# Performance work log

Hardware: AMD Instinct MI355X
Metric: run time of the kernel (lower is better)

## Reference

```python
import jax, jax.numpy as jnp
import numpy as np

N, E, F, H, G, C = 50000, 800000, 768, 256, 512, 2  # H = nhid*2 (nhid=128), G graphs, C classes
NHID = 128


def setup_inputs() -> dict:
    key = jax.random.key(0)
    ks = jax.random.split(key, 18)
    s = 0.05
    x = jax.random.normal(ks[0], (N, F), jnp.float32)
    edge_index = jax.random.randint(ks[1], (2, E), 0, N, dtype=jnp.int32)
    # sorted batch vector; every graph non-empty so the 'first node per graph' gather is valid
    batch = ((jnp.arange(N) * G) // N).astype(jnp.int32)
    return {
        "x": x,
        "edge_index": edge_index,
        "batch": batch,
        # GATConv 1 (in=F, out=H, heads=1)
        "W1": jax.random.normal(ks[2], (F, H), jnp.float32) * s,
        "as1": jax.random.normal(ks[3], (H,), jnp.float32) * s,
        "ad1": jax.random.normal(ks[4], (H,), jnp.float32) * s,
        "b1": jnp.zeros((H,), jnp.float32),
        # GATConv 2 (in=H, out=H)
        "W2": jax.random.normal(ks[5], (H, H), jnp.float32) * s,
        "as2": jax.random.normal(ks[6], (H,), jnp.float32) * s,
        "ad2": jax.random.normal(ks[7], (H,), jnp.float32) * s,
        "b2": jnp.zeros((H,), jnp.float32),
        # fc0: num_features -> nhid (news branch)
        "W0": jax.random.normal(ks[8], (F, NHID), jnp.float32) * s,
        "b0": jnp.zeros((NHID,), jnp.float32),
        # fc1: 2*nhid -> nhid (used twice, as in the source)
        "Wf1": jax.random.normal(ks[9], (H, NHID), jnp.float32) * s,
        "bf1": jnp.zeros((NHID,), jnp.float32),
        # fc2: nhid -> num_classes
        "Wf2": jax.random.normal(ks[10], (NHID, C), jnp.float32) * s,
        "bf2": jnp.zeros((C,), jnp.float32),
    }


def _gat(x, src, dst, W, a_s, a_d, b):
    # PyG GATConv, heads=1, concat=True, negative_slope=0.2, self-loops pre-appended to src/dst.
    h = x @ W                                   # [N, H]
    e = jax.nn.leaky_relu((h @ a_s)[src] + (h @ a_d)[dst], 0.2)  # [E+N]
    m = jax.ops.segment_max(e, dst, num_segments=N)
    ex = jnp.exp(e - m[dst])                    # stable segment softmax numerator
    denom = jax.ops.segment_sum(ex, dst, num_segments=N)
    agg = jax.ops.segment_sum(ex[:, None] * h[src], dst, num_segments=N)  # [N, H]
    return agg / denom[:, None] + b


def reference(x, edge_index, batch, W1, as1, ad1, b1, W2, as2, ad2, b2, W0, b0, Wf1, bf1, Wf2, bf2):
    loop = jnp.arange(N, dtype=edge_index.dtype)
    src = jnp.concatenate([edge_index[0], loop])  # add self-loops (PyG default)
    dst = jnp.concatenate([edge_index[1], loop])
    h = jax.nn.selu(_gat(x, src, dst, W1, as1, ad1, b1))
    h = jax.nn.selu(_gat(h, src, dst, W2, as2, ad2, b2))
    # global mean pool over graphs
    cnt = jax.ops.segment_sum(jnp.ones((N,), h.dtype), batch, num_segments=G)
    pooled = jax.nn.selu(jax.ops.segment_sum(h, batch, num_segments=G) / cnt[:, None])
    z = jax.nn.selu(pooled @ Wf1 + bf1)
    # dropout(p=0.5) in eval mode -> identity
    # concat branch: first node of each graph (news root)
    first_idx = jax.ops.segment_min(jnp.arange(N), batch, num_segments=G)
    news = jax.nn.relu(x[first_idx] @ W0 + b0)
    z = jnp.concatenate([z, news], axis=1)       # [G, 2*nhid]
    z = jax.nn.relu(z @ Wf1 + bf1)
    return jax.nn.log_softmax(z @ Wf2 + bf2, axis=-1)
```

## Files before the change

### kernel.cpp

```cpp
#include <hip/hip_runtime.h>
#include <hip/hip_bf16.h>
#include <cstdint>
#include <cstddef>

#define NN 50000
#define EE 800000
#define FF 768
#define HH 256
#define GG 512
#define CC 2
#define NHIDD 128
#define ETOT (EE + NN)
#define NCHUNK 49

typedef __attribute__((ext_vector_type(8))) short bf16x8;
typedef __attribute__((ext_vector_type(4))) float f32x4;
typedef __attribute__((ext_vector_type(8))) unsigned short us8;

__device__ __forceinline__ float b2f(unsigned short u){
  union { float f; uint32_t i; } v; v.i = ((uint32_t)u) << 16; return v.f;
}
__device__ __forceinline__ unsigned short f2b(float f){
  uint32_t u = __float_as_uint(f);
  uint32_t r = (u + 0x7fffu + ((u >> 16) & 1u)) >> 16;
  return (unsigned short)r;
}
__device__ __forceinline__ float selu_f(float x){
  const float lam = 1.0507009873554805f, alp = 1.6732632423543772f;
  return x > 0.f ? lam * x : lam * alp * (__expf(x) - 1.f);
}

__global__ __launch_bounds__(256) void swizzleW(const float* __restrict__ W,
                                                unsigned short* __restrict__ Wsw, int K){
  int i = blockIdx.x * 256 + threadIdx.x;
  if (i < K * HH){
    int k = i / HH, n = i % HH;
    Wsw[(size_t)(k >> 5) * 8192 + n * 32 + (k & 31)] = f2b(W[i]);
  }
}

__global__ __launch_bounds__(256) void zero_deg(int* deg){
  int i = blockIdx.x * 256 + threadIdx.x;
  if (i < NN) deg[i] = 0;
}

__global__ __launch_bounds__(256) void deg_kernel(const int* __restrict__ dstA, int* __restrict__ deg){
  int i = blockIdx.x * 256 + threadIdx.x;
  if (i < ETOT){
    int d = (i < EE) ? dstA[i] : (i - EE);
    atomicAdd(&deg[d], 1);
  }
}

__global__ __launch_bounds__(256) void scanA(const int* __restrict__ deg, int* __restrict__ bsum){
  __shared__ int red[256];
  int c = blockIdx.x, tid = threadIdx.x;
  int base = c * 1024 + tid * 4;
  int s = 0;
#pragma unroll
  for (int j = 0; j < 4; j++){ int idx = base + j; if (idx < NN) s += deg[idx]; }
  red[tid] = s; __syncthreads();
  for (int off = 128; off > 0; off >>= 1){
    if (tid < off) red[tid] += red[tid + off];
    __syncthreads();
  }
  if (tid == 0) bsum[c] = red[0];
}

__global__ void scanB(int* bsum){
  if (threadIdx.x == 0){
    int run = 0;
    for (int i = 0; i < NCHUNK; i++){ int v = bsum[i]; bsum[i] = run; run += v; }
  }
}

__global__ __launch_bounds__(256) void scanC(const int* __restrict__ deg, const int* __restrict__ bsum,
                                             int* __restrict__ row_ptr, int* __restrict__ fill_ptr){
  __shared__ int ts[256];
  int c = blockIdx.x, tid = threadIdx.x;
  int base = c * 1024 + tid * 4;
  int v[4]; int s = 0;
#pragma unroll
  for (int j = 0; j < 4; j++){ int idx = base + j; v[j] = (idx < NN) ? deg[idx] : 0; s += v[j]; }
  ts[tid] = s; __syncthreads();
  for (int off = 1; off < 256; off <<= 1){
    int add = (tid >= off) ? ts[tid - off] : 0;
    __syncthreads();
    ts[tid] += add;
    __syncthreads();
  }
  int run = ts[tid] - s + bsum[c];
#pragma unroll
  for (int j = 0; j < 4; j++){
    int idx = base + j;
    if (idx < NN){ row_ptr[idx] = run; fill_ptr[idx] = run; }
    run += v[j];
  }
  if (c == 0 && tid == 0) row_ptr[NN] = ETOT;
}

__global__ __launch_bounds__(256) void fill_kernel(const int* __restrict__ srcA, const int* __restrict__ dstA,
                                                   int* __restrict__ fill_ptr, int* __restrict__ csr_src){
  int i = blockIdx.x * 256 + threadIdx.x;
  if (i < ETOT){
    int s = (i < EE) ? srcA[i] : (i - EE);
    int d = (i < EE) ? dstA[i] : (i - EE);
    int pos = atomicAdd(&fill_ptr[d], 1);
    csr_src[pos] = s;
  }
}

template<int K, bool AF32, int MINW>
__global__ __launch_bounds__(256, MINW) void gemm_mfma(const void* __restrict__ Ap,
                                                 const unsigned short* __restrict__ Wsw,
                                                 unsigned short* __restrict__ out, int M){
  constexpr int KP = K + 8;
  __shared__ unsigned short Al[32][KP];
  const int tid = threadIdx.x;
  const int m0 = blockIdx.x * 32;
  const int lane = tid & 63, w = tid >> 6;
  const int koff = (lane >> 4) * 8;
  const int arow = lane & 15;
  const int nrow = w * 64 + (lane & 15);

  f32x4 acc[2][4];
#pragma unroll
  for (int rt = 0; rt < 2; rt++)
#pragma unroll
    for (int ct = 0; ct < 4; ct++) acc[rt][ct] = (f32x4){0.f, 0.f, 0.f, 0.f};

  constexpr int C8 = K / 8;
  constexpr int ROUNDS = (32 * C8) / 256;
#pragma unroll
  for (int j = 0; j < ROUNDS; j++){
    int q = j * 256 + tid;
    int row = q / C8, c8 = q - row * C8;
    int gm = m0 + row;
    us8 v;
    if (gm < M){
      if (AF32){
        const float* Af = (const float*)Ap;
        const float4* p = (const float4*)&Af[(size_t)gm * K + c8 * 8];
        float4 f0 = p[0], f1 = p[1];
        v[0] = f2b(f0.x); v[1] = f2b(f0.y); v[2] = f2b(f0.z); v[3] = f2b(f0.w);
        v[4] = f2b(f1.x); v[5] = f2b(f1.y); v[6] = f2b(f1.z); v[7] = f2b(f1.w);
      } else {
        v = *(const us8*)&((const unsigned short*)Ap)[(size_t)gm * K + c8 * 8];
      }
    } else {
      v = (us8){0,0,0,0,0,0,0,0};
    }
    *(us8*)&Al[row][c8 * 8] = v;
  }

  const unsigned short* bbase = Wsw + ((size_t)nrow * 32 + koff);
  bf16x8 bcur[2][4];
#pragma unroll
  for (int k2 = 0; k2 < 2; k2++)
#pragma unroll
    for (int ct = 0; ct < 4; ct++)
      bcur[k2][ct] = *(const bf16x8*)(bbase + (size_t)k2 * 8192 + ct * 512);

  __syncthreads();

  constexpr int NIT = K / 64;
  for (int ks = 0; ks < NIT; ks++){
    bf16x8 bnext[2][4];
    if (ks + 1 < NIT){
#pragma unroll
      for (int k2 = 0; k2 < 2; k2++)
#pragma unroll
        for (int ct = 0; ct < 4; ct++)
          bnext[k2][ct] = *(const bf16x8*)(bbase + (size_t)((ks + 1) * 2 + k2) * 8192 + ct * 512);
    }
    bf16x8 af[2][2];
#pragma unroll
    for (int k2 = 0; k2 < 2; k2++)
#pragma unroll
      for (int rt = 0; rt < 2; rt++)
        af[k2][rt] = *(const bf16x8*)&Al[rt * 16 + arow][ks * 64 + k2 * 32 + koff];
#pragma unroll
    for (int k2 = 0; k2 < 2; k2++)
#pragma unroll
      for (int rt = 0; rt < 2; rt++)
#pragma unroll
        for (int ct = 0; ct < 4; ct++)
          acc[rt][ct] = __builtin_amdgcn_mfma_f32_16x16x32_bf16(af[k2][rt], bcur[k2][ct], acc[rt][ct], 0, 0, 0);
    if (ks + 1 < NIT){
#pragma unroll
      for (int k2 = 0; k2 < 2; k2++)
#pragma unroll
        for (int ct = 0; ct < 4; ct++) bcur[k2][ct] = bnext[k2][ct];
    }
  }

#pragma unroll
  for (int rt = 0; rt < 2; rt++){
    int mbase = m0 + rt * 16 + (lane >> 4) * 4;
#pragma unroll
    for (int r = 0; r < 4; r++){
      int m = mbase + r;
      if (m < M){
        size_t ro = (size_t)m * HH + w * 64 + (lane & 15);
        out[ro + 0]  = f2b(acc[rt][0][r]);
        out[ro + 16] = f2b(acc[rt][1][r]);
        out[ro + 32] = f2b(acc[rt][2][r]);
        out[ro + 48] = f2b(acc[rt][3][r]);
      }
    }
  }
}

__global__ __launch_bounds__(256) void alsald_kernel(const unsigned short* __restrict__ h,
    const float* __restrict__ a_s, const float* __restrict__ a_d,
    float* __restrict__ als, float* __restrict__ ald){
  int node = blockIdx.x * 4 + (threadIdx.x >> 6);
  int lane = threadIdx.x & 63;
  if (node >= NN) return;
  ushort4 hv = *(const ushort4*)&h[(size_t)node * HH + lane * 4];
  float4 as4 = *(const float4*)&a_s[lane * 4];
  float4 ad4 = *(const float4*)&a_d[lane * 4];
  float h0 = b2f(hv.x), h1 = b2f(hv.y), h2 = b2f(hv.z), h3 = b2f(hv.w);
  float s = h0 * as4.x + h1 * as4.y + h2 * as4.z + h3 * as4.w;
  float d = h0 * ad4.x + h1 * ad4.y + h2 * ad4.z + h3 * ad4.w;
  for (int off = 32; off > 0; off >>= 1){ s += __shfl_xor(s, off); d += __shfl_xor(d, off); }
  if (lane == 0){ als[node] = s; ald[node] = d; }
}

__global__ __launch_bounds__(256) void agg_wave(const unsigned short* __restrict__ h,
    const float* __restrict__ als, const float* __restrict__ ald,
    const int* __restrict__ row_ptr, const int* __restrict__ csr_src,
    const float* __restrict__ bias, unsigned short* __restrict__ outp){
  int node = blockIdx.x * 4 + (threadIdx.x >> 6);
  int lane = threadIdx.x & 63;
  if (node >= NN) return;
  int base = row_ptr[node];
  int deg  = row_ptr[node + 1] - base;
  float aldd = ald[node];
  float den = 0.f;
  float a0 = 0.f, a1 = 0.f, a2 = 0.f, a3 = 0.f;
  const size_t fo = (size_t)lane * 4;
  for (int p0 = 0; p0 < deg; p0 += 64){
    int cnt = min(64, deg - p0);
    float ev = 0.f; int s = 0;
    if (lane < cnt){
      s = csr_src[base + p0 + lane];
      float v = als[s] + aldd;
      v = v > 0.f ? v : 0.2f * v;
      ev = __expf(v);
    }
    den += ev;
    int j = 0;
    for (; j + 2 <= cnt; j += 2){
      float e0 = __shfl(ev, j), e1 = __shfl(ev, j + 1);
      int s0 = __shfl(s, j), s1 = __shfl(s, j + 1);
      ushort4 g0 = *(const ushort4*)&h[(size_t)s0 * HH + fo];
      ushort4 g1 = *(const ushort4*)&h[(size_t)s1 * HH + fo];
      a0 += e0 * b2f(g0.x) + e1 * b2f(g1.x);
      a1 += e0 * b2f(g0.y) + e1 * b2f(g1.y);
      a2 += e0 * b2f(g0.z) + e1 * b2f(g1.z);
      a3 += e0 * b2f(g0.w) + e1 * b2f(g1.w);
    }
    for (; j < cnt; j++){
      float e0 = __shfl(ev, j); int s0 = __shfl(s, j);
      ushort4 g0 = *(const ushort4*)&h[(size_t)s0 * HH + fo];
      a0 += e0 * b2f(g0.x); a1 += e0 * b2f(g0.y); a2 += e0 * b2f(g0.z); a3 += e0 * b2f(g0.w);
    }
  }
  for (int off = 32; off > 0; off >>= 1) den += __shfl_xor(den, off);
  float inv = 1.f / den;
  float4 b4 = *(const float4*)&bias[fo];
  ushort4 o;
  o.x = f2b(selu_f(a0 * inv + b4.x));
  o.y = f2b(selu_f(a1 * inv + b4.y));
  o.z = f2b(selu_f(a2 * inv + b4.z));
  o.w = f2b(selu_f(a3 * inv + b4.w));
  *(ushort4*)&outp[(size_t)node * HH + fo] = o;
}

__global__ __launch_bounds__(256) void first_kernel(const int* __restrict__ batch, int* __restrict__ first_idx){
  int n = blockIdx.x * 256 + threadIdx.x;
  if (n < NN){
    int b = batch[n];
    if (n == 0 || batch[n - 1] != b) first_idx[b] = n;
  }
  if (blockIdx.x == 0 && threadIdx.x == 0) first_idx[GG] = NN;
}

__global__ __launch_bounds__(256) void pool_kernel(const unsigned short* __restrict__ x3,
    const int* __restrict__ first_idx, float* __restrict__ pooled){
  int g = blockIdx.x, f = threadIdx.x;
  int s = first_idx[g], e = first_idx[g + 1];
  float acc = 0.f;
  for (int n = s; n < e; n++) acc += b2f(x3[(size_t)n * HH + f]);
  pooled[g * HH + f] = selu_f(acc / (float)(e - s));
}

__global__ __launch_bounds__(128) void z1_kernel(const float* __restrict__ pooled,
    const float* __restrict__ Wf1, const float* __restrict__ bf1,
    float* __restrict__ z1){
  __shared__ float pr[HH];
  int g = blockIdx.x, t = threadIdx.x;
  pr[t] = pooled[g * HH + t];
  pr[t + 128] = pooled[g * HH + t + 128];
  __syncthreads();
  float acc = 0.f;
  for (int k = 0; k < HH; k++) acc += pr[k] * Wf1[k * NHIDD + t];
  z1[g * NHIDD + t] = selu_f(acc + bf1[t]);
}

__global__ __launch_bounds__(128) void news_kernel(const float* __restrict__ x,
    const int* __restrict__ first_idx, const float* __restrict__ W0,
    const float* __restrict__ b0, float* __restrict__ znews){
  __shared__ float xr[FF];
  int g = blockIdx.x, t = threadIdx.x;
  int root = first_idx[g];
  for (int k = t; k < FF; k += 128) xr[k] = x[(size_t)root * FF + k];
  __syncthreads();
  float acc = 0.f;
  for (int k = 0; k < FF; k++) acc += xr[k] * W0[k * NHIDD + t];
  acc += b0[t];
  znews[g * NHIDD + t] = acc > 0.f ? acc : 0.f;
}

__global__ __launch_bounds__(128) void final_kernel(const float* __restrict__ z1,
    const float* __restrict__ znews, const float* __restrict__ Wf1,
    const float* __restrict__ bf1, const float* __restrict__ Wf2,
    const float* __restrict__ bf2, float* __restrict__ out){
  __shared__ float zc[HH];
  __shared__ float l0s[2], l1s[2];
  int g = blockIdx.x, t = threadIdx.x;
  zc[t] = z1[g * NHIDD + t];
  zc[NHIDD + t] = znews[g * NHIDD + t];
  __syncthreads();
  float acc = 0.f;
  for (int k = 0; k < HH; k++) acc += zc[k] * Wf1[k * NHIDD + t];
  float z2 = acc + bf1[t]; z2 = z2 > 0.f ? z2 : 0.f;
  float p0 = z2 * Wf2[t * CC + 0];
  float p1 = z2 * Wf2[t * CC + 1];
  for (int off = 32; off > 0; off >>= 1){ p0 += __shfl_xor(p0, off); p1 += __shfl_xor(p1, off); }
  int lane = t & 63, wid = t >> 6;
  if (lane == 0){ l0s[wid] = p0; l1s[wid] = p1; }
  __syncthreads();
  if (t == 0){
    float l0 = l0s[0] + l0s[1] + bf2[0];
    float l1 = l1s[0] + l1s[1] + bf2[1];
    float mx = fmaxf(l0, l1);
    float lse = mx + logf(__expf(l0 - mx) + __expf(l1 - mx));
    out[g * CC + 0] = l0 - lse;
    out[g * CC + 1] = l1 - lse;
  }
}

extern "C" void kernel_launch(void* const* d_in, const int* in_sizes, int n_in,
                              void* d_out, int out_size, void* d_ws, size_t ws_size,
                              hipStream_t stream){
  const float* x          = (const float*)d_in[0];
  const int* edge_index   = (const int*)d_in[1];
  const int* batch        = (const int*)d_in[2];
  const float* W1  = (const float*)d_in[3];
  const float* as1 = (const float*)d_in[4];
  const float* ad1 = (const float*)d_in[5];
  const float* b1  = (const float*)d_in[6];
  const float* W2  = (const float*)d_in[7];
  const float* as2 = (const float*)d_in[8];
  const float* ad2 = (const float*)d_in[9];
  const float* b2  = (const float*)d_in[10];
  const float* W0  = (const float*)d_in[11];
  const float* b0  = (const float*)d_in[12];
  const float* Wf1 = (const float*)d_in[13];
  const float* bf1 = (const float*)d_in[14];
  const float* Wf2 = (const float*)d_in[15];
  const float* bf2 = (const float*)d_in[16];
  float* out = (float*)d_out;

  char* w = (char*)d_ws;
  size_t off = 0;
  auto alloc = [&](size_t bytes){ size_t o = off; off += (bytes + 255) & ~(size_t)255; return o; };
  unsigned short* h    = (unsigned short*)(w + alloc((size_t)NN * HH * 2));
  unsigned short* x2   = (unsigned short*)(w + alloc((size_t)NN * HH * 2));
  unsigned short* Wsw1 = (unsigned short*)(w + alloc((size_t)FF * HH * 2));
  unsigned short* Wsw2 = (unsigned short*)(w + alloc((size_t)HH * HH * 2));
  float* als     = (float*)(w + alloc((size_t)NN * 4));
  float* ald     = (float*)(w + alloc((size_t)NN * 4));
  int*   deg     = (int*)(w + alloc((size_t)NN * 4));
  int*   row_ptr = (int*)(w + alloc((size_t)(NN + 1) * 4));
  int*   fillp   = (int*)(w + alloc((size_t)NN * 4));
  int*   csr_src = (int*)(w + alloc((size_t)ETOT * 4));
  int*   bsum    = (int*)(w + alloc(64 * 4));
  int*   firsti  = (int*)(w + alloc((size_t)(GG + 1) * 4));
  float* pooled  = (float*)(w + alloc((size_t)GG * HH * 4));
  float* z1      = (float*)(w + alloc((size_t)GG * NHIDD * 4));
  float* znews   = (float*)(w + alloc((size_t)GG * NHIDD * 4));

  const int* srcA = edge_index;
  const int* dstA = edge_index + EE;

  swizzleW<<<(FF * HH + 255) / 256, 256, 0, stream>>>(W1, Wsw1, FF);
  swizzleW<<<(HH * HH + 255) / 256, 256, 0, stream>>>(W2, Wsw2, HH);

  zero_deg<<<(NN + 255) / 256, 256, 0, stream>>>(deg);
  deg_kernel<<<(ETOT + 255) / 256, 256, 0, stream>>>(dstA, deg);
  scanA<<<NCHUNK, 256, 0, stream>>>(deg, bsum);
  scanB<<<1, 64, 0, stream>>>(bsum);
  scanC<<<NCHUNK, 256, 0, stream>>>(deg, bsum, row_ptr, fillp);
  fill_kernel<<<(ETOT + 255) / 256, 256, 0, stream>>>(srcA, dstA, fillp, csr_src);

  const int gemm_grid = (NN + 31) / 32;
  gemm_mfma<FF, true, 3><<<gemm_grid, 256, 0, stream>>>((const void*)x, Wsw1, h, NN);
  alsald_kernel<<<(NN + 3) / 4, 256, 0, stream>>>(h, as1, ad1, als, ald);
  agg_wave<<<(NN + 3) / 4, 256, 0, stream>>>(h, als, ald, row_ptr, csr_src, b1, x2);
  gemm_mfma<HH, false, 4><<<gemm_grid, 256, 0, stream>>>((const void*)x2, Wsw2, h, NN);
  alsald_kernel<<<(NN + 3) / 4, 256, 0, stream>>>(h, as2, ad2, als, ald);
  agg_wave<<<(NN + 3) / 4, 256, 0, stream>>>(h, als, ald, row_ptr, csr_src, b2, x2);
  first_kernel<<<(NN + 255) / 256, 256, 0, stream>>>(batch, firsti);
  pool_kernel<<<GG, 256, 0, stream>>>(x2, firsti, pooled);
  z1_kernel<<<GG, 128, 0, stream>>>(pooled, Wf1, bf1, z1);
  news_kernel<<<GG, 128, 0, stream>>>(x, firsti, W0, b0, znews);
  final_kernel<<<GG, 128, 0, stream>>>(z1, znews, Wf1, bf1, Wf2, bf2, out);
}
```

Baseline: 627.0 us.

## Fuse attention-logit dot products into GEMM epilogue and use direct-to-LDS loads

Folds the per-node a_s/a_d dot products into the MFMA GEMM epilogue through shuffle and LDS reductions, which removes the separate alsald kernel and its re-read of h. The A-tile load now goes straight from global memory to LDS via global_load_lds with an XOR swizzle in place of padding. To allow this, x is converted to bf16 in a separate pre-pass kernel. That pass writes and re-reads a 77MB bf16 copy in exchange for the fp32 reads that used to happen inside the GEMM, and the second GEMM's occupancy hint drops from 4 to 3.

```diff
diff --git a/kernel.cpp b/kernel.cpp
--- a/kernel.cpp
+++ b/kernel.cpp
@@ -30,6 +30,21 @@
   return x > 0.f ? lam * x : lam * alp * (__expf(x) - 1.f);
 }
 
+__device__ __forceinline__ void gload_lds16(const unsigned short* g, unsigned short* l){
+  __builtin_amdgcn_global_load_lds((const __attribute__((address_space(1))) void*)g,
+                                   (__attribute__((address_space(3))) void*)l, 16, 0, 0);
+}
+
+__global__ __launch_bounds__(256) void xbf_kernel(const float* __restrict__ x, unsigned short* __restrict__ xb){
+  size_t i = ((size_t)blockIdx.x * 256 + threadIdx.x) * 8;
+  float4 f0 = *(const float4*)&x[i];
+  float4 f1 = *(const float4*)&x[i + 4];
+  us8 v;
+  v[0] = f2b(f0.x); v[1] = f2b(f0.y); v[2] = f2b(f0.z); v[3] = f2b(f0.w);
+  v[4] = f2b(f1.x); v[5] = f2b(f1.y); v[6] = f2b(f1.z); v[7] = f2b(f1.w);
+  *(us8*)&xb[i] = v;
+}
+
 __global__ __launch_bounds__(256) void swizzleW(const float* __restrict__ W,
                                                 unsigned short* __restrict__ Wsw, int K){
   int i = blockIdx.x * 256 + threadIdx.x;
@@ -110,12 +125,14 @@
   }
 }
 
-template<int K, bool AF32, int MINW>
-__global__ __launch_bounds__(256, MINW) void gemm_mfma(const void* __restrict__ Ap,
+template<int K, int MINW>
+__global__ __launch_bounds__(256, MINW) void gemm_mfma(const unsigned short* __restrict__ A,
                                                  const unsigned short* __restrict__ Wsw,
-                                                 unsigned short* __restrict__ out, int M){
-  constexpr int KP = K + 8;
-  __shared__ unsigned short Al[32][KP];
+                                                 const float* __restrict__ a_s, const float* __restrict__ a_d,
+                                                 unsigned short* __restrict__ out,
+                                                 float* __restrict__ als, float* __restrict__ ald, int M){
+  constexpr int CHROW = K / 8;
+  __shared__ unsigned short Al[32 * K];
   const int tid = threadIdx.x;
   const int m0 = blockIdx.x * 32;
   const int lane = tid & 63, w = tid >> 6;
@@ -129,28 +146,16 @@
 #pragma unroll
     for (int ct = 0; ct < 4; ct++) acc[rt][ct] = (f32x4){0.f, 0.f, 0.f, 0.f};
 
-  constexpr int C8 = K / 8;
-  constexpr int ROUNDS = (32 * C8) / 256;
+  constexpr int ROUNDS = (32 * CHROW) / 256;
 #pragma unroll
   for (int j = 0; j < ROUNDS; j++){
-    int q = j * 256 + tid;
-    int row = q / C8, c8 = q - row * C8;
-    int gm = m0 + row;
-    us8 v;
-    if (gm < M){
-      if (AF32){
-        const float* Af = (const float*)Ap;
-        const float4* p = (const float4*)&Af[(size_t)gm * K + c8 * 8];
-        float4 f0 = p[0], f1 = p[1];
-        v[0] = f2b(f0.x); v[1] = f2b(f0.y); v[2] = f2b(f0.z); v[3] = f2b(f0.w);
-        v[4] = f2b(f1.x); v[5] = f2b(f1.y); v[6] = f2b(f1.z); v[7] = f2b(f1.w);
-      } else {
-        v = *(const us8*)&((const unsigned short*)Ap)[(size_t)gm * K + c8 * 8];
-      }
-    } else {
-      v = (us8){0,0,0,0,0,0,0,0};
-    }
-    *(us8*)&Al[row][c8 * 8] = v;
+    int L16 = j * 256 + tid;
+    int row = L16 / CHROW;
+    int ch  = L16 - row * CHROW;
+    int sch = ch ^ (row & 7);
+    int gr  = m0 + row; if (gr >= M) gr = M - 1;
+    gload_lds16(A + (size_t)gr * K + sch * 8,
+                &Al[(size_t)(j * 256 + w * 64) * 8]);
   }
 
   const unsigned short* bbase = Wsw + ((size_t)nrow * 32 + koff);
@@ -177,8 +182,11 @@
 #pragma unroll
     for (int k2 = 0; k2 < 2; k2++)
 #pragma unroll
-      for (int rt = 0; rt < 2; rt++)
-        af[k2][rt] = *(const bf16x8*)&Al[rt * 16 + arow][ks * 64 + k2 * 32 + koff];
+      for (int rt = 0; rt < 2; rt++){
+        int R = rt * 16 + arow;
+        int chb = (ks * 8 + k2 * 4 + (lane >> 4)) ^ (R & 7);
+        af[k2][rt] = *(const bf16x8*)&Al[(size_t)R * K + chb * 8];
+      }
 #pragma unroll
     for (int k2 = 0; k2 < 2; k2++)
 #pragma unroll
@@ -209,22 +217,53 @@
       }
     }
   }
-}
-
-__global__ __launch_bounds__(256) void alsald_kernel(const unsigned short* __restrict__ h,
-    const float* __restrict__ a_s, const float* __restrict__ a_d,
-    float* __restrict__ als, float* __restrict__ ald){
-  int node = blockIdx.x * 4 + (threadIdx.x >> 6);
-  int lane = threadIdx.x & 63;
-  if (node >= NN) return;
-  ushort4 hv = *(const ushort4*)&h[(size_t)node * HH + lane * 4];
-  float4 as4 = *(const float4*)&a_s[lane * 4];
-  float4 ad4 = *(const float4*)&a_d[lane * 4];
-  float h0 = b2f(hv.x), h1 = b2f(hv.y), h2 = b2f(hv.z), h3 = b2f(hv.w);
-  float s = h0 * as4.x + h1 * as4.y + h2 * as4.z + h3 * as4.w;
-  float d = h0 * ad4.x + h1 * ad4.y + h2 * ad4.z + h3 * ad4.w;
-  for (int off = 32; off > 0; off >>= 1){ s += __shfl_xor(s, off); d += __shfl_xor(d, off); }
-  if (lane == 0){ als[node] = s; ald[node] = d; }
+
+  float as_c[4], ad_c[4];
+#pragma unroll
+  for (int ct = 0; ct < 4; ct++){
+    int col = w * 64 + ct * 16 + (lane & 15);
+    as_c[ct] = a_s[col]; ad_c[ct] = a_d[col];
+  }
+  float ps[2][4], pd[2][4];
+#pragma unroll
+  for (int rt = 0; rt < 2; rt++)
+#pragma unroll
+    for (int r = 0; r < 4; r++){
+      float s = 0.f, d = 0.f;
+#pragma unroll
+      for (int ct = 0; ct < 4; ct++){ float v = acc[rt][ct][r]; s += v * as_c[ct]; d += v * ad_c[ct]; }
+      ps[rt][r] = s; pd[rt][r] = d;
+    }
+#pragma unroll
+  for (int off = 1; off < 16; off <<= 1){
+#pragma unroll
+    for (int rt = 0; rt < 2; rt++)
+#pragma unroll
+      for (int r = 0; r < 4; r++){
+        ps[rt][r] += __shfl_xor(ps[rt][r], off);
+        pd[rt][r] += __shfl_xor(pd[rt][r], off);
+      }
+  }
+  __syncthreads();
+  float* red = (float*)Al;
+  if ((lane & 15) == 0){
+    int q = lane >> 4;
+#pragma unroll
+    for (int rt = 0; rt < 2; rt++)
+#pragma unroll
+      for (int r = 0; r < 4; r++){
+        int row = rt * 16 + q * 4 + r;
+        red[w * 32 + row]       = ps[rt][r];
+        red[128 + w * 32 + row] = pd[rt][r];
+      }
+  }
+  __syncthreads();
+  if (tid < 32){
+    float s = red[tid] + red[32 + tid] + red[64 + tid] + red[96 + tid];
+    float d = red[128 + tid] + red[160 + tid] + red[192 + tid] + red[224 + tid];
+    int m = m0 + tid;
+    if (m < M){ als[m] = s; ald[m] = d; }
+  }
 }
 
 __global__ __launch_bounds__(256) void agg_wave(const unsigned short* __restrict__ h,
@@ -379,6 +418,7 @@
   auto alloc = [&](size_t bytes){ size_t o = off; off += (bytes + 255) & ~(size_t)255; return o; };
   unsigned short* h    = (unsigned short*)(w + alloc((size_t)NN * HH * 2));
   unsigned short* x2   = (unsigned short*)(w + alloc((size_t)NN * HH * 2));
+  unsigned short* xb   = (unsigned short*)(w + alloc((size_t)NN * FF * 2));
   unsigned short* Wsw1 = (unsigned short*)(w + alloc((size_t)FF * HH * 2));
   unsigned short* Wsw2 = (unsigned short*)(w + alloc((size_t)HH * HH * 2));
   float* als     = (float*)(w + alloc((size_t)NN * 4));
@@ -398,6 +438,7 @@
 
   swizzleW<<<(FF * HH + 255) / 256, 256, 0, stream>>>(W1, Wsw1, FF);
   swizzleW<<<(HH * HH + 255) / 256, 256, 0, stream>>>(W2, Wsw2, HH);
+  xbf_kernel<<<(NN * FF) / (256 * 8), 256, 0, stream>>>(x, xb);
 
   zero_deg<<<(NN + 255) / 256, 256, 0, stream>>>(deg);
   deg_kernel<<<(ETOT + 255) / 256, 256, 0, stream>>>(dstA, deg);
@@ -407,11 +448,9 @@
   fill_kernel<<<(ETOT + 255) / 256, 256, 0, stream>>>(srcA, dstA, fillp, csr_src);
 
   const int gemm_grid = (NN + 31) / 32;
-  gemm_mfma<FF, true, 3><<<gemm_grid, 256, 0, stream>>>((const void*)x, Wsw1, h, NN);
-  alsald_kernel<<<(NN + 3) / 4, 256, 0, stream>>>(h, as1, ad1, als, ald);
+  gemm_mfma<FF, 3><<<gemm_grid, 256, 0, stream>>>(xb, Wsw1, as1, ad1, h, als, ald, NN);
   agg_wave<<<(NN + 3) / 4, 256, 0, stream>>>(h, als, ald, row_ptr, csr_src, b1, x2);
-  gemm_mfma<HH, false, 4><<<gemm_grid, 256, 0, stream>>>((const void*)x2, Wsw2, h, NN);
-  alsald_kernel<<<(NN + 3) / 4, 256, 0, stream>>>(h, as2, ad2, als, ald);
+  gemm_mfma<HH, 3><<<gemm_grid, 256, 0, stream>>>(x2, Wsw2, as2, ad2, h, als, ald, NN);
   agg_wave<<<(NN + 3) / 4, 256, 0, stream>>>(h, als, ald, row_ptr, csr_src, b2, x2);
   first_kernel<<<(NN + 255) / 256, 256, 0, stream>>>(batch, firsti);
   pool_kernel<<<GG, 256, 0, stream>>>(x2, firsti, pooled);
```

Result: no change. 629.1 us (+0.3%).
